# Kernel tuning notes

Hardware: AMD Instinct MI355X
Metric: run time of the kernel (lower is better)

## Reference

```python
import jax, jax.numpy as jnp
import numpy as np
import math

G, NPG, D = 64, 2048, 128   # graphs, nodes per graph, feature dim
DEG = 16
N = G * NPG
E = N * DEG
VOCAB = 100000
RATIO = 0.8


def setup_inputs() -> dict:
    key = jax.random.key(0)
    ks = jax.random.split(key, 24)
    node_ids = jax.random.randint(ks[0], (N, 1), 0, VOCAB)
    # within-graph edges: endpoints in [0, NPG) per graph, then add graph offset
    within = jax.random.randint(ks[1], (2, G, NPG * DEG), 0, NPG)
    offs = (jnp.arange(G) * NPG)[None, :, None]
    edge_index = (within + offs).reshape(2, E)
    batch = jnp.repeat(jnp.arange(G), NPG)
    f = lambda k, shape: jax.random.normal(k, shape, dtype=jnp.float32) * 0.05
    return dict(
        node_ids=node_ids, edge_index=edge_index, batch=batch,
        emb=f(ks[2], (VOCAB, D)),
        Wl1=f(ks[3], (D, D)), Wr1=f(ks[4], (D, D)), bl1=f(ks[5], (D,)), pw1=f(ks[6], (D,)),
        Wl2=f(ks[7], (D, D)), Wr2=f(ks[8], (D, D)), bl2=f(ks[9], (D,)), pw2=f(ks[10], (D,)),
        Wl3=f(ks[11], (D, D)), Wr3=f(ks[12], (D, D)), bl3=f(ks[13], (D,)), pw3=f(ks[14], (D,)),
        W1=f(ks[15], (128, 256)), b1=f(ks[16], (128,)),
        W2=f(ks[17], (64, 128)), b2=f(ks[18], (64,)),
        W3=f(ks[19], (1, 64)), b3=f(ks[20], (1,)),
    )


def sage(x, src, dst, emask, Wl, bl, Wr):
    # PyG SAGEConv (mean aggr): lin_l(mean_j x_j) + lin_r(x_i); lin_r has no bias
    n = x.shape[0]
    msg = x[src] * emask[:, None].astype(x.dtype)
    dstm = jnp.where(emask, dst, n)  # dummy segment for invalid edges
    s = jax.ops.segment_sum(msg, dstm, num_segments=n + 1)[:n]
    c = jax.ops.segment_sum(emask.astype(x.dtype), dstm, num_segments=n + 1)[:n]
    mean = s / jnp.maximum(c, 1.0)[:, None]
    return mean @ Wl.T + bl + x @ Wr.T


def topk_pool(x, src, dst, emask, w, n_per):
    # PyG TopKPooling: score = tanh(x.w/||w||), keep top ceil(ratio*n) per graph,
    # scale kept features by score, remap/filter edges.
    n = x.shape[0]
    g = n // n_per
    k = math.ceil(RATIO * n_per)
    score = jnp.tanh((x @ w) / jnp.linalg.norm(w))
    ts, ti = jax.lax.top_k(score.reshape(g, n_per), k)  # [g, k]
    perm = (ti + (jnp.arange(g) * n_per)[:, None]).reshape(-1)  # old global idx
    x_new = x[perm] * ts.reshape(-1)[:, None]
    n_new = g * k
    new_of_old = jnp.full((n,), n_new, dtype=jnp.int32).at[perm].set(
        jnp.arange(n_new, dtype=jnp.int32))
    sn, dn = new_of_old[src], new_of_old[dst]
    em = emask & (sn < n_new) & (dn < n_new)
    sn = jnp.where(em, sn, 0)
    dn = jnp.where(em, dn, n_new)
    return x_new, sn, dn, em, k


def readout(x, k):
    # cat([global_max_pool, global_mean_pool]) with equal-size graphs
    g = x.shape[0] // k
    xr = x.reshape(g, k, -1)
    return jnp.concatenate([xr.max(axis=1), xr.mean(axis=1)], axis=1)


def reference(node_ids, edge_index, batch, emb,
              Wl1, Wr1, bl1, pw1, Wl2, Wr2, bl2, pw2, Wl3, Wr3, bl3, pw3,
              W1, b1, W2, b2, W3, b3):
    x = emb[node_ids.squeeze(1)]                       # [N, 128]
    src, dst = edge_index[0], edge_index[1]
    em = jnp.ones((src.shape[0],), dtype=bool)

    x = jax.nn.relu(sage(x, src, dst, em, Wl1, bl1, Wr1))
    x, src, dst, em, k1 = topk_pool(x, src, dst, em, pw1, NPG)
    x1 = readout(x, k1)

    x = jax.nn.relu(sage(x, src, dst, em, Wl2, bl2, Wr2))
    x, src, dst, em, k2 = topk_pool(x, src, dst, em, pw2, k1)
    x2 = readout(x, k2)

    x = jax.nn.relu(sage(x, src, dst, em, Wl3, bl3, Wr3))
    x, src, dst, em, k3 = topk_pool(x, src, dst, em, pw3, k2)
    x3 = readout(x, k3)

    h = x1 + x2 + x3                                   # [G, 256]
    h = jax.nn.relu(h @ W1.T + b1)
    h = jax.nn.relu(h @ W2.T + b2)                     # dropout = identity (eval)
    return jax.nn.sigmoid(h @ W3.T + b3).squeeze(1)    # [G]
```

## Files before the change

### kernel.cpp

```cpp
#include <hip/hip_runtime.h>
#include <hip/hip_bf16.h>
#include <float.h>

typedef _Float16 f16x8 __attribute__((ext_vector_type(8)));
typedef float f32x4 __attribute__((ext_vector_type(4)));

#define GRAPHS 64
#define NPG 2048
#define DIM 128
#define NNODES (GRAPHS * NPG)
#define NEDGES (NNODES * 16)
#define ECAP 32768
#define NSB 8
#define RPB 256

__global__ __launch_bounds__(256) void embed_kernel(const int* __restrict__ ids,
    const float* __restrict__ emb, _Float16* __restrict__ xh) {
  int idx = blockIdx.x * 256 + threadIdx.x;
  int nd = idx >> 4, part = idx & 15;
  int id = ids[nd];
  const float* src = emb + (size_t)id * 128 + part * 8;
  float4 a = *(const float4*)(src);
  float4 b = *(const float4*)(src + 4);
  f16x8 o;
  o[0] = (_Float16)a.x; o[1] = (_Float16)a.y; o[2] = (_Float16)a.z; o[3] = (_Float16)a.w;
  o[4] = (_Float16)b.x; o[5] = (_Float16)b.y; o[6] = (_Float16)b.z; o[7] = (_Float16)b.w;
  *(f16x8*)(xh + (size_t)nd * 128 + part * 8) = o;
}

__global__ __launch_bounds__(256) void convert_w(const float* __restrict__ Wl,
    const float* __restrict__ Wr, _Float16* __restrict__ wh) {
  int qq = blockIdx.x * 256 + threadIdx.x;
  int ks = qq >> 9, nf = (qq >> 6) & 7, l = qq & 63;
  int ncol = nf * 16 + (l & 15);
  int k0 = (ks & 3) * 32 + ((l >> 4) << 3);
  const float* wsrc = ((ks < 4) ? Wl : Wr) + ncol * 128 + k0;
  float4 a = *(const float4*)wsrc;
  float4 b = *(const float4*)(wsrc + 4);
  f16x8 w;
  w[0] = (_Float16)a.x; w[1] = (_Float16)a.y; w[2] = (_Float16)a.z; w[3] = (_Float16)a.w;
  w[4] = (_Float16)b.x; w[5] = (_Float16)b.y; w[6] = (_Float16)b.z; w[7] = (_Float16)b.w;
  *(f16x8*)(wh + (size_t)qq * 8) = w;
}

__global__ __launch_bounds__(1024) void csr_hist(const int* __restrict__ src,
    const int* __restrict__ dst, int np, int* __restrict__ part) {
  __shared__ int hist[2048];
  int x = blockIdx.x;
  int s = x & 7, q = x >> 3;
  int b = q & (NSB - 1), gh = q >> 3;
  int g = gh * 8 + s;
  int tid = threadIdx.x;
  for (int i = tid; i < 2048; i += 1024) hist[i] = 0;
  __syncthreads();
  int e0 = g * ECAP + b * (ECAP / NSB);
  int nodebase = g * np;
  for (int e = tid; e < ECAP / NSB; e += 1024) {
    atomicAdd(&hist[dst[e0 + e] - nodebase], 1);
  }
  __syncthreads();
  for (int i = tid; i < np; i += 1024) part[((size_t)(g * NSB + b)) * 2048 + i] = hist[i];
}

__global__ __launch_bounds__(1024) void csr_scan(const int* __restrict__ part, int np,
    int* __restrict__ offb, int* __restrict__ deg, int* __restrict__ curs) {
  __shared__ int psum[1024];
  int g = blockIdx.x, tid = threadIdx.x;
  int i0 = 2 * tid, i1 = 2 * tid + 1;
  int p0[NSB], p1[NSB];
  int c0 = 0, c1 = 0;
#pragma unroll
  for (int b = 0; b < NSB; ++b) {
    p0[b] = (i0 < np) ? part[((size_t)(g * NSB + b)) * 2048 + i0] : 0;
    p1[b] = (i1 < np) ? part[((size_t)(g * NSB + b)) * 2048 + i1] : 0;
    c0 += p0[b]; c1 += p1[b];
  }
  int pair = c0 + c1;
  psum[tid] = pair;
  for (int s = 1; s < 1024; s <<= 1) {
    __syncthreads();
    int t = (tid >= s) ? psum[tid - s] : 0;
    __syncthreads();
    psum[tid] += t;
  }
  int excl = psum[tid] - pair;
  int ebase = g * ECAP;
  int nodebase = g * np;
  if (i0 < np) {
    int off = ebase + excl;
    offb[nodebase + i0] = off;
    deg[nodebase + i0] = c0;
    int cur = off;
#pragma unroll
    for (int b = 0; b < NSB; ++b) { curs[((size_t)(g * NSB + b)) * 2048 + i0] = cur; cur += p0[b]; }
  }
  if (i1 < np) {
    int off = ebase + excl + c0;
    offb[nodebase + i1] = off;
    deg[nodebase + i1] = c1;
    int cur = off;
#pragma unroll
    for (int b = 0; b < NSB; ++b) { curs[((size_t)(g * NSB + b)) * 2048 + i1] = cur; cur += p1[b]; }
  }
}

__global__ __launch_bounds__(1024) void csr_place(const int* __restrict__ src,
    const int* __restrict__ dst, int np, const int* __restrict__ curs,
    int* __restrict__ esort) {
  __shared__ int cur[2048];
  int x = blockIdx.x;
  int s = x & 7, q = x >> 3;
  int b = q & (NSB - 1), gh = q >> 3;
  int g = gh * 8 + s;
  int tid = threadIdx.x;
  for (int i = tid; i < np; i += 1024) cur[i] = curs[((size_t)(g * NSB + b)) * 2048 + i];
  __syncthreads();
  int e0 = g * ECAP + b * (ECAP / NSB);
  int nodebase = g * np;
  for (int e = tid; e < ECAP / NSB; e += 1024) {
    int ge = e0 + e;
    int p = atomicAdd(&cur[dst[ge] - nodebase], 1);
    esort[p] = src[ge];
  }
}

__global__ __launch_bounds__(256) void remap_esort(const int* __restrict__ esort0,
    const int* __restrict__ noo, int* __restrict__ esortl, int E4) {
  int t = blockIdx.x * 256 + threadIdx.x;
  if (t >= E4) return;
  int4 s = *(const int4*)(esort0 + t * 4);
  int4 o;
  o.x = noo[s.x]; o.y = noo[s.y]; o.z = noo[s.z]; o.w = noo[s.w];
  *(int4*)(esortl + t * 4) = o;
}

__global__ __launch_bounds__(256) void aggregate_kernel(const _Float16* __restrict__ xh,
    const int* __restrict__ offb, const int* __restrict__ deg, const int* __restrict__ esrc,
    _Float16* __restrict__ meanh, int np, int C) {
  int bid = blockIdx.x;
  int s = bid & 7, q = bid >> 3;
  int gsub = q / C, chunk = q - gsub * C;
  int g = gsub * 8 + s;
  int wave = threadIdx.x >> 6, lane = threadIdx.x & 63;
  int sub = lane >> 4, l = lane & 15;
  int local = chunk * 16 + wave * 4 + sub;
  if (local >= np) return;
  int w = g * np + local;
  int b = offb[w], c = deg[w];
  int e = b + c;
  float acc[8] = {0.f, 0.f, 0.f, 0.f, 0.f, 0.f, 0.f, 0.f};
  int i = b;
  for (; i + 4 <= e; i += 4) {
    int s0 = esrc[i], s1 = esrc[i + 1], s2 = esrc[i + 2], s3 = esrc[i + 3];
    f16x8 v0 = *(const f16x8*)(xh + (size_t)s0 * 128 + l * 8);
    f16x8 v1 = *(const f16x8*)(xh + (size_t)s1 * 128 + l * 8);
    f16x8 v2 = *(const f16x8*)(xh + (size_t)s2 * 128 + l * 8);
    f16x8 v3 = *(const f16x8*)(xh + (size_t)s3 * 128 + l * 8);
    f16x8 t = (v0 + v1) + (v2 + v3);
#pragma unroll
    for (int j = 0; j < 8; ++j) acc[j] += (float)t[j];
  }
  for (; i < e; ++i) {
    int srcn = esrc[i];
    f16x8 v = *(const f16x8*)(xh + (size_t)srcn * 128 + l * 8);
#pragma unroll
    for (int j = 0; j < 8; ++j) acc[j] += (float)v[j];
  }
  float inv = 1.f / (float)(c > 0 ? c : 1);
  f16x8 o;
#pragma unroll
  for (int j = 0; j < 8; ++j) o[j] = (_Float16)(acc[j] * inv);
  *(f16x8*)(meanh + (size_t)w * 128 + l * 8) = o;
}

__global__ __launch_bounds__(256) void aggregate_f(const _Float16* __restrict__ xh,
    const int* __restrict__ offb0, const int* __restrict__ deg0, const int* __restrict__ esortl,
    const int* __restrict__ orig, _Float16* __restrict__ meanh, int np, int C) {
  int bid = blockIdx.x;
  int s = bid & 7, q = bid >> 3;
  int gsub = q / C, chunk = q - gsub * C;
  int g = gsub * 8 + s;
  int wave = threadIdx.x >> 6, lane = threadIdx.x & 63;
  int sub = lane >> 4, l = lane & 15;
  int local = chunk * 16 + wave * 4 + sub;
  if (local >= np) return;
  int w = g * np + local;
  int o = orig[w];
  int b = offb0[o], c0 = deg0[o];
  int e = b + c0;
  float acc[8] = {0.f, 0.f, 0.f, 0.f, 0.f, 0.f, 0.f, 0.f};
  int cnt = 0;
  const f16x8 zero = {(_Float16)0.f, (_Float16)0.f, (_Float16)0.f, (_Float16)0.f,
                      (_Float16)0.f, (_Float16)0.f, (_Float16)0.f, (_Float16)0.f};
  int i = b;
  for (; i + 4 <= e; i += 4) {
    int n0 = esortl[i], n1 = esortl[i + 1], n2 = esortl[i + 2], n3 = esortl[i + 3];
    f16x8 v0 = zero, v1 = zero, v2 = zero, v3 = zero;
    if (n0 >= 0) v0 = *(const f16x8*)(xh + (size_t)n0 * 128 + l * 8);
    if (n1 >= 0) v1 = *(const f16x8*)(xh + (size_t)n1 * 128 + l * 8);
    if (n2 >= 0) v2 = *(const f16x8*)(xh + (size_t)n2 * 128 + l * 8);
    if (n3 >= 0) v3 = *(const f16x8*)(xh + (size_t)n3 * 128 + l * 8);
    cnt += (n0 >= 0) + (n1 >= 0) + (n2 >= 0) + (n3 >= 0);
    f16x8 t = (v0 + v1) + (v2 + v3);
#pragma unroll
    for (int j = 0; j < 8; ++j) acc[j] += (float)t[j];
  }
  for (; i < e; ++i) {
    int sn = esortl[i];
    if (sn < 0) continue;
    ++cnt;
    f16x8 v = *(const f16x8*)(xh + (size_t)sn * 128 + l * 8);
#pragma unroll
    for (int j = 0; j < 8; ++j) acc[j] += (float)v[j];
  }
  float inv = 1.f / (float)(cnt > 0 ? cnt : 1);
  f16x8 ov;
#pragma unroll
  for (int j = 0; j < 8; ++j) ov[j] = (_Float16)(acc[j] * inv);
  *(f16x8*)(meanh + (size_t)w * 128 + l * 8) = ov;
}

__global__ __launch_bounds__(256, 2) void sage_gemm(const _Float16* __restrict__ XH,
    const _Float16* MEANIN, _Float16* OUT, const _Float16* __restrict__ WH,
    const float* __restrict__ bl, const float* __restrict__ pw, float* __restrict__ sc,
    int n) {
  __shared__ _Float16 WB[4096 * 8];
  int tid = threadIdx.x;
  for (int qq = tid; qq < 4096; qq += 256)
    *(f16x8*)(WB + qq * 8) = *(const f16x8*)(WH + (size_t)qq * 8);
  __syncthreads();
  int wave = tid >> 6, lane = tid & 63;
  int wrow0 = blockIdx.x * RPB + wave * 64;
  if (wrow0 >= n) return;
  int kb = (lane >> 4) << 3;
  int lr = lane & 15;
  f32x4 acc[4][8];
#pragma unroll
  for (int t = 0; t < 4; ++t)
#pragma unroll
    for (int nf = 0; nf < 8; ++nf) acc[t][nf] = (f32x4){0.f, 0.f, 0.f, 0.f};
#pragma unroll
  for (int ks = 0; ks < 8; ++ks) {
    const _Float16* A = (ks < 4) ? MEANIN : XH;
    const _Float16* ap = A + (size_t)(wrow0 + lr) * 128 + (ks & 3) * 32 + kb;
    f16x8 a0 = *(const f16x8*)(ap);
    f16x8 a1 = *(const f16x8*)(ap + 16 * 128);
    f16x8 a2 = *(const f16x8*)(ap + 32 * 128);
    f16x8 a3 = *(const f16x8*)(ap + 48 * 128);
#pragma unroll
    for (int nf = 0; nf < 8; ++nf) {
      f16x8 b = *(const f16x8*)(WB + ((ks * 8 + nf) * 64 + lane) * 8);
      acc[0][nf] = __builtin_amdgcn_mfma_f32_16x16x32_f16(a0, b, acc[0][nf], 0, 0, 0);
      acc[1][nf] = __builtin_amdgcn_mfma_f32_16x16x32_f16(a1, b, acc[1][nf], 0, 0, 0);
      acc[2][nf] = __builtin_amdgcn_mfma_f32_16x16x32_f16(a2, b, acc[2][nf], 0, 0, 0);
      acc[3][nf] = __builtin_amdgcn_mfma_f32_16x16x32_f16(a3, b, acc[3][nf], 0, 0, 0);
    }
  }
  float pwv[8], qn = 0.f;
#pragma unroll
  for (int nf = 0; nf < 8; ++nf) {
    pwv[nf] = pw[nf * 16 + lr];
    qn += pwv[nf] * pwv[nf];
  }
#pragma unroll
  for (int o = 1; o < 16; o <<= 1) qn += __shfl_xor(qn, o);
  float inv_n = 1.f / sqrtf(qn);
#pragma unroll
  for (int t = 0; t < 4; ++t) {
    int rbase = wrow0 + t * 16 + ((lane >> 4) << 2);
    float dot[4] = {0.f, 0.f, 0.f, 0.f};
#pragma unroll
    for (int nf = 0; nf < 8; ++nf) {
      int col = nf * 16 + lr;
      float bias = bl[col];
#pragma unroll
      for (int r = 0; r < 4; ++r) {
        float v = fmaxf(acc[t][nf][r] + bias, 0.f);
        OUT[(size_t)(rbase + r) * 128 + col] = (_Float16)v;
        dot[r] += v * pwv[nf];
      }
    }
#pragma unroll
    for (int r = 0; r < 4; ++r) {
#pragma unroll
      for (int o = 1; o < 16; o <<= 1) dot[r] += __shfl_xor(dot[r], o);
    }
    if (lr == 0) {
#pragma unroll
      for (int r = 0; r < 4; ++r) sc[rbase + r] = tanhf(dot[r] * inv_n);
    }
  }
}

__global__ __launch_bounds__(1024) void topk_fused(const float* __restrict__ sc,
    int n_per, int k, const _Float16* __restrict__ meanin, _Float16* __restrict__ xh,
    int* __restrict__ nooA, const int* __restrict__ orig_in, int* __restrict__ orig_out,
    float* __restrict__ h, int mode) {
  __shared__ unsigned long long L[2048];
  __shared__ int c2n[2048];
  __shared__ float redmax[2048];
  __shared__ float redsum[2048];
  int g = blockIdx.x;
  int tid = threadIdx.x;
  int lane = tid & 63, wave = tid >> 6;
  int i0 = wave * 128 + lane;
  int i1 = i0 + 64;
  const float* scg = sc + g * n_per;
  auto keyize = [&](int i) -> unsigned long long {
    float f = (i < n_per) ? scg[i] : -FLT_MAX;
    unsigned u = __float_as_uint(f);
    u = (u & 0x80000000u) ? ~u : (u | 0x80000000u);
    return ((unsigned long long)u << 32) | (unsigned)(2047 - i);
  };
  unsigned long long a = keyize(i0), b = keyize(i1);
#pragma clang loop unroll(disable)
  for (unsigned kk = 2; kk <= 2048; kk <<= 1) {
#pragma clang loop unroll(disable)
    for (unsigned j = kk >> 1; j >= 128; j >>= 1) {
      L[i0] = a; L[i1] = b;
      __syncthreads();
      unsigned long long pa = L[i0 ^ j], pb = L[i1 ^ j];
      bool dA = ((i0 & kk) == 0), lA = ((i0 & j) == 0);
      if ((dA == lA) ? (pa > a) : (pa < a)) a = pa;
      bool dB = ((i1 & kk) == 0), lB = ((i1 & j) == 0);
      if ((dB == lB) ? (pb > b) : (pb < b)) b = pb;
      __syncthreads();
    }
    if (kk >= 128) {
      bool desc = ((i0 & kk) == 0);
      if ((a < b) == desc) { unsigned long long t = a; a = b; b = t; }
    }
    unsigned jtop = (kk >> 1 < 32u) ? (kk >> 1) : 32u;
#pragma clang loop unroll(disable)
    for (unsigned j = jtop; j >= 1; j >>= 1) {
      unsigned long long oa = __shfl_xor(a, (int)j);
      unsigned long long ob = __shfl_xor(b, (int)j);
      bool low = ((lane & j) == 0);
      bool dA = ((i0 & kk) == 0);
      if ((dA == low) ? (oa > a) : (oa < a)) a = oa;
      bool dB = ((i1 & kk) == 0);
      if ((dB == low) ? (ob > b) : (ob < b)) b = ob;
    }
  }
  L[i0] = a; L[i1] = b;
  int orig_a = 2047 - (int)(a & 0xFFFFFFFFu);
  int orig_b = 2047 - (int)(b & 0xFFFFFFFFu);
  if (mode == 0) {
    if (orig_a < n_per) nooA[g * n_per + orig_a] = (i0 < k) ? g * k + i0 : -1;
    if (orig_b < n_per) nooA[g * n_per + orig_b] = (i1 < k) ? g * k + i1 : -1;
  } else if (mode == 1) {
    if (orig_a < n_per) c2n[orig_a] = (i0 < k) ? g * k + i0 : -1;
    if (orig_b < n_per) c2n[orig_b] = (i1 < k) ? g * k + i1 : -1;
  }
  __syncthreads();
  if (mode == 1) {
    for (int o2 = tid; o2 < NPG; o2 += 1024) {
      int a0 = nooA[g * NPG + o2];
      nooA[g * NPG + o2] = (a0 >= 0) ? c2n[a0 - g * n_per] : -1;
    }
  }
  int grp = tid >> 4, l8 = tid & 15;
  float vmax[8], vsum[8];
#pragma unroll
  for (int j = 0; j < 8; ++j) { vmax[j] = -FLT_MAX; vsum[j] = 0.f; }
  for (int r = grp; r < k; r += 64) {
    unsigned long long key = L[r];
    int orig = 2047 - (int)(key & 0xFFFFFFFFu);
    int p = g * n_per + orig;
    float score = scg[orig];
    f16x8 v = *(const f16x8*)(meanin + (size_t)p * 128 + l8 * 8);
    f16x8 ovv;
#pragma unroll
    for (int j = 0; j < 8; ++j) {
      float val = (float)v[j] * score;
      ovv[j] = (_Float16)val;
      vmax[j] = fmaxf(vmax[j], val);
      vsum[j] += val;
    }
    *(f16x8*)(xh + (size_t)(g * k + r) * 128 + l8 * 8) = ovv;
    if (l8 == 0) orig_out[g * k + r] = orig_in ? orig_in[p] : p;
  }
#pragma unroll
  for (int j = 0; j < 8; ++j) {
    vmax[j] = fmaxf(vmax[j], __shfl_xor(vmax[j], 16));
    vmax[j] = fmaxf(vmax[j], __shfl_xor(vmax[j], 32));
    vsum[j] += __shfl_xor(vsum[j], 16);
    vsum[j] += __shfl_xor(vsum[j], 32);
  }
  if ((lane >> 4) == 0) {
#pragma unroll
    for (int j = 0; j < 8; ++j) {
      redmax[wave * 128 + l8 * 8 + j] = vmax[j];
      redsum[wave * 128 + l8 * 8 + j] = vsum[j];
    }
  }
  __syncthreads();
  if (tid < 128) {
    float m = -FLT_MAX, s2 = 0.f;
#pragma unroll
    for (int wv = 0; wv < 16; ++wv) {
      m = fmaxf(m, redmax[wv * 128 + tid]);
      s2 += redsum[wv * 128 + tid];
    }
    h[g * 256 + tid] += m;
    h[g * 256 + 128 + tid] += s2 / (float)k;
  }
}

__global__ __launch_bounds__(256) void mlp1(const float* __restrict__ h, const float* __restrict__ W1,
    const float* __restrict__ b1, float* __restrict__ h1) {
  int o = blockIdx.x * 256 + threadIdx.x;
  int g = o >> 7, j = o & 127;
  const float* hp = h + g * 256;
  const float* wp = W1 + j * 256;
  float a = b1[j];
  for (int c = 0; c < 256; ++c) a += hp[c] * wp[c];
  h1[o] = fmaxf(a, 0.f);
}

__global__ __launch_bounds__(256) void mlp2(const float* __restrict__ h1, const float* __restrict__ W2,
    const float* __restrict__ b2, float* __restrict__ h2) {
  int o = blockIdx.x * 256 + threadIdx.x;
  int g = o >> 6, j = o & 63;
  const float* hp = h1 + g * 128;
  const float* wp = W2 + j * 128;
  float a = b2[j];
  for (int c = 0; c < 128; ++c) a += hp[c] * wp[c];
  h2[o] = fmaxf(a, 0.f);
}

__global__ __launch_bounds__(64) void mlp3(const float* __restrict__ h2, const float* __restrict__ W3,
    const float* __restrict__ b3, float* __restrict__ out) {
  int g = threadIdx.x;
  if (g >= 64) return;
  const float* hp = h2 + g * 64;
  float a = b3[0];
  for (int c = 0; c < 64; ++c) a += hp[c] * W3[c];
  out[g] = 1.f / (1.f + expf(-a));
}

extern "C" void kernel_launch(void* const* d_in, const int* in_sizes, int n_in,
                              void* d_out, int out_size, void* d_ws, size_t ws_size,
                              hipStream_t stream) {
  const int* node_ids = (const int*)d_in[0];
  const int* ei = (const int*)d_in[1];
  const float* emb = (const float*)d_in[3];
  const float* W[3][4] = {
      {(const float*)d_in[4], (const float*)d_in[5], (const float*)d_in[6], (const float*)d_in[7]},
      {(const float*)d_in[8], (const float*)d_in[9], (const float*)d_in[10], (const float*)d_in[11]},
      {(const float*)d_in[12], (const float*)d_in[13], (const float*)d_in[14], (const float*)d_in[15]}};
  const float* W1 = (const float*)d_in[16];
  const float* b1 = (const float*)d_in[17];
  const float* W2 = (const float*)d_in[18];
  const float* b2 = (const float*)d_in[19];
  const float* W3 = (const float*)d_in[20];
  const float* b3 = (const float*)d_in[21];
  float* out = (float*)d_out;

  const int E = NEDGES;
  char* ws = (char*)d_ws;
  size_t o = 0;
  auto alloc = [&](size_t bytes) { void* p = ws + o; o = (o + bytes + 255) & ~(size_t)255; return p; };
  _Float16* XH = (_Float16*)alloc((size_t)NNODES * 128 * 2);
  _Float16* MEANH = (_Float16*)alloc((size_t)NNODES * 128 * 2);
  int* ESORT = (int*)alloc((size_t)E * 4);
  int* ESORTL = (int*)alloc((size_t)E * 4);
  int* PART = (int*)alloc((size_t)GRAPHS * NSB * 2048 * 4);
  int* CURS = (int*)alloc((size_t)GRAPHS * NSB * 2048 * 4);
  int* OFFB = (int*)alloc((size_t)NNODES * 4);
  int* DEG = (int*)alloc((size_t)NNODES * 4);
  float* SC = (float*)alloc((size_t)NNODES * 4);
  int* NOOA = (int*)alloc((size_t)NNODES * 4);
  int* ORIGA = (int*)alloc((size_t)NNODES * 4);
  int* ORIGB = (int*)alloc((size_t)NNODES * 4);
  _Float16* WH0 = (_Float16*)alloc(4096 * 8 * 2);
  _Float16* WH1 = (_Float16*)alloc(4096 * 8 * 2);
  _Float16* WH2 = (_Float16*)alloc(4096 * 8 * 2);
  float* H = (float*)alloc(64 * 256 * 4);
  float* H1 = (float*)alloc(64 * 128 * 4);
  float* H2 = (float*)alloc(64 * 64 * 4);

  embed_kernel<<<NNODES * 16 / 256, 256, 0, stream>>>(node_ids, emb, XH);
  hipMemsetAsync(H, 0, 64 * 256 * 4, stream);
  convert_w<<<16, 256, 0, stream>>>(W[0][0], W[0][1], WH0);
  convert_w<<<16, 256, 0, stream>>>(W[1][0], W[1][1], WH1);
  convert_w<<<16, 256, 0, stream>>>(W[2][0], W[2][1], WH2);

  const int* src = ei;
  const int* dst = ei + E;
  csr_hist<<<GRAPHS * NSB, 1024, 0, stream>>>(src, dst, NPG, PART);
  csr_scan<<<GRAPHS, 1024, 0, stream>>>(PART, NPG, OFFB, DEG, CURS);
  csr_place<<<GRAPHS * NSB, 1024, 0, stream>>>(src, dst, NPG, CURS, ESORT);

  struct LayerP { int n, k; };
  LayerP L[3] = {{131072, 1639}, {104896, 1312}, {83968, 1050}};
  _Float16* WHs[3] = {WH0, WH1, WH2};
  int* ORIG_cur = ORIGA;
  int* ORIG_next = ORIGB;

  for (int li = 0; li < 3; ++li) {
    int n = L[li].n, k = L[li].k;
    int np = n / 64;
    const float *bl = W[li][2], *pw = W[li][3];

    int C = (np + 15) / 16;
    if (li == 0) {
      aggregate_kernel<<<64 * C, 256, 0, stream>>>(XH, OFFB, DEG, ESORT, MEANH, np, C);
    } else {
      remap_esort<<<E / 4 / 256, 256, 0, stream>>>(ESORT, NOOA, ESORTL, E / 4);
      aggregate_f<<<64 * C, 256, 0, stream>>>(XH, OFFB, DEG, ESORTL, ORIG_cur,
                                              MEANH, np, C);
    }
    sage_gemm<<<(n + RPB - 1) / RPB, 256, 0, stream>>>(XH, MEANH, MEANH, WHs[li], bl, pw, SC, n);
    topk_fused<<<GRAPHS, 1024, 0, stream>>>(SC, np, k, MEANH, XH, NOOA,
        (li == 0) ? nullptr : ORIG_cur, ORIG_next, H, li);
    { int* t = ORIG_cur; ORIG_cur = ORIG_next; ORIG_next = t; }
  }

  mlp1<<<32, 256, 0, stream>>>(H, W1, b1, H1);
  mlp2<<<16, 256, 0, stream>>>(H1, W2, b2, H2);
  mlp3<<<1, 64, 0, stream>>>(H2, W3, b3, out);
}
```

Measured before the change: 367.7 us.

## Split top-k pooling into sort, parallel gather/readout, and combine kernels

Result: no change. 363.4 us (-1.2%).

```diff
diff --git a/kernel.cpp b/kernel.cpp
--- a/kernel.cpp
+++ b/kernel.cpp
@@ -12,6 +12,7 @@
 #define NEDGES (NNODES * 16)
 #define ECAP 32768
 #define NSB 8
+#define RSL 8
 #define RPB 256
 
 __global__ __launch_bounds__(256) void embed_kernel(const int* __restrict__ ids,
@@ -292,14 +293,10 @@
   }
 }
 
-__global__ __launch_bounds__(1024) void topk_fused(const float* __restrict__ sc,
-    int n_per, int k, const _Float16* __restrict__ meanin, _Float16* __restrict__ xh,
-    int* __restrict__ nooA, const int* __restrict__ orig_in, int* __restrict__ orig_out,
-    float* __restrict__ h, int mode) {
+__global__ __launch_bounds__(1024) void topk_sort(const float* __restrict__ sc,
+    int n_per, int k, int* __restrict__ nooA, int* __restrict__ rankt, int mode) {
   __shared__ unsigned long long L[2048];
   __shared__ int c2n[2048];
-  __shared__ float redmax[2048];
-  __shared__ float redsum[2048];
   int g = blockIdx.x;
   int tid = threadIdx.x;
   int lane = tid & 63, wave = tid >> 6;
@@ -342,30 +339,40 @@
       if ((dB == low) ? (ob > b) : (ob < b)) b = ob;
     }
   }
-  L[i0] = a; L[i1] = b;
   int orig_a = 2047 - (int)(a & 0xFFFFFFFFu);
   int orig_b = 2047 - (int)(b & 0xFFFFFFFFu);
+  if (i0 < k) rankt[g * NPG + i0] = orig_a;
+  if (i1 < k) rankt[g * NPG + i1] = orig_b;
   if (mode == 0) {
     if (orig_a < n_per) nooA[g * n_per + orig_a] = (i0 < k) ? g * k + i0 : -1;
     if (orig_b < n_per) nooA[g * n_per + orig_b] = (i1 < k) ? g * k + i1 : -1;
   } else if (mode == 1) {
     if (orig_a < n_per) c2n[orig_a] = (i0 < k) ? g * k + i0 : -1;
     if (orig_b < n_per) c2n[orig_b] = (i1 < k) ? g * k + i1 : -1;
-  }
-  __syncthreads();
-  if (mode == 1) {
+    __syncthreads();
     for (int o2 = tid; o2 < NPG; o2 += 1024) {
       int a0 = nooA[g * NPG + o2];
       nooA[g * NPG + o2] = (a0 >= 0) ? c2n[a0 - g * n_per] : -1;
     }
   }
-  int grp = tid >> 4, l8 = tid & 15;
+}
+
+__global__ __launch_bounds__(256) void topk_tail(const float* __restrict__ sc,
+    const int* __restrict__ rankt, int n_per, int k, const _Float16* __restrict__ meanin,
+    _Float16* __restrict__ xh, const int* __restrict__ orig_in, int* __restrict__ orig_out,
+    float* __restrict__ pmax, float* __restrict__ psum) {
+  int g = blockIdx.x >> 3;
+  int slice = blockIdx.x & (RSL - 1);
+  int rpb = (k + RSL - 1) / RSL;
+  int r0 = slice * rpb;
+  int r1 = r0 + rpb; if (r1 > k) r1 = k;
+  const float* scg = sc + g * n_per;
+  int grp = threadIdx.x >> 4, l8 = threadIdx.x & 15;
   float vmax[8], vsum[8];
 #pragma unroll
   for (int j = 0; j < 8; ++j) { vmax[j] = -FLT_MAX; vsum[j] = 0.f; }
-  for (int r = grp; r < k; r += 64) {
-    unsigned long long key = L[r];
-    int orig = 2047 - (int)(key & 0xFFFFFFFFu);
+  for (int r = r0 + grp; r < r1; r += 16) {
+    int orig = rankt[g * NPG + r];
     int p = g * n_per + orig;
     float score = scg[orig];
     f16x8 v = *(const f16x8*)(meanin + (size_t)p * 128 + l8 * 8);
@@ -380,6 +387,8 @@
     *(f16x8*)(xh + (size_t)(g * k + r) * 128 + l8 * 8) = ovv;
     if (l8 == 0) orig_out[g * k + r] = orig_in ? orig_in[p] : p;
   }
+  __shared__ float smax[4 * 128], ssum[4 * 128];
+  int lane = threadIdx.x & 63, wave = threadIdx.x >> 6;
 #pragma unroll
   for (int j = 0; j < 8; ++j) {
     vmax[j] = fmaxf(vmax[j], __shfl_xor(vmax[j], 16));
@@ -390,21 +399,32 @@
   if ((lane >> 4) == 0) {
 #pragma unroll
     for (int j = 0; j < 8; ++j) {
-      redmax[wave * 128 + l8 * 8 + j] = vmax[j];
-      redsum[wave * 128 + l8 * 8 + j] = vsum[j];
+      smax[wave * 128 + l8 * 8 + j] = vmax[j];
+      ssum[wave * 128 + l8 * 8 + j] = vsum[j];
     }
   }
   __syncthreads();
-  if (tid < 128) {
-    float m = -FLT_MAX, s2 = 0.f;
-#pragma unroll
-    for (int wv = 0; wv < 16; ++wv) {
-      m = fmaxf(m, redmax[wv * 128 + tid]);
-      s2 += redsum[wv * 128 + tid];
-    }
-    h[g * 256 + tid] += m;
-    h[g * 256 + 128 + tid] += s2 / (float)k;
-  }
+  if (threadIdx.x < 128) {
+    int d = threadIdx.x;
+    float m = fmaxf(fmaxf(smax[d], smax[128 + d]), fmaxf(smax[256 + d], smax[384 + d]));
+    float s2 = ssum[d] + ssum[128 + d] + ssum[256 + d] + ssum[384 + d];
+    pmax[(size_t)(g * RSL + slice) * 128 + d] = m;
+    psum[(size_t)(g * RSL + slice) * 128 + d] = s2;
+  }
+}
+
+__global__ __launch_bounds__(256) void readout_comb(const float* __restrict__ pmax,
+    const float* __restrict__ psum, int k, float* __restrict__ h) {
+  int idx = blockIdx.x * 256 + threadIdx.x;
+  int g = idx >> 7, d = idx & 127;
+  float vmax = -FLT_MAX, vs = 0.f;
+#pragma unroll
+  for (int s = 0; s < RSL; ++s) {
+    vmax = fmaxf(vmax, pmax[(size_t)(g * RSL + s) * 128 + d]);
+    vs += psum[(size_t)(g * RSL + s) * 128 + d];
+  }
+  h[g * 256 + d] += vmax;
+  h[g * 256 + 128 + d] += vs / (float)k;
 }
 
 __global__ __launch_bounds__(256) void mlp1(const float* __restrict__ h, const float* __restrict__ W1,
@@ -471,11 +491,14 @@
   int* DEG = (int*)alloc((size_t)NNODES * 4);
   float* SC = (float*)alloc((size_t)NNODES * 4);
   int* NOOA = (int*)alloc((size_t)NNODES * 4);
+  int* RANKT = (int*)alloc((size_t)NNODES * 4);
   int* ORIGA = (int*)alloc((size_t)NNODES * 4);
   int* ORIGB = (int*)alloc((size_t)NNODES * 4);
   _Float16* WH0 = (_Float16*)alloc(4096 * 8 * 2);
   _Float16* WH1 = (_Float16*)alloc(4096 * 8 * 2);
   _Float16* WH2 = (_Float16*)alloc(4096 * 8 * 2);
+  float* PMAX = (float*)alloc((size_t)GRAPHS * RSL * 128 * 4);
+  float* PSUM = (float*)alloc((size_t)GRAPHS * RSL * 128 * 4);
   float* H = (float*)alloc(64 * 256 * 4);
   float* H1 = (float*)alloc(64 * 128 * 4);
   float* H2 = (float*)alloc(64 * 64 * 4);
@@ -512,8 +535,10 @@
                                               MEANH, np, C);
     }
     sage_gemm<<<(n + RPB - 1) / RPB, 256, 0, stream>>>(XH, MEANH, MEANH, WHs[li], bl, pw, SC, n);
-    topk_fused<<<GRAPHS, 1024, 0, stream>>>(SC, np, k, MEANH, XH, NOOA,
-        (li == 0) ? nullptr : ORIG_cur, ORIG_next, H, li);
+    topk_sort<<<GRAPHS, 1024, 0, stream>>>(SC, np, k, NOOA, RANKT, li);
+    topk_tail<<<GRAPHS * RSL, 256, 0, stream>>>(SC, RANKT, np, k, MEANH, XH,
+        (li == 0) ? nullptr : ORIG_cur, ORIG_next, PMAX, PSUM);
+    readout_comb<<<32, 256, 0, stream>>>(PMAX, PSUM, k, H);
     { int* t = ORIG_cur; ORIG_cur = ORIG_next; ORIG_next = t; }
   }
 
```
